# Optimization experiments

Hardware: AMD Instinct MI355X
Metric: run time of the kernel (lower is better)

The kernel has to match this reference:

```python
import jax, jax.numpy as jnp
import numpy as np

D = 192          # embed_dim
DI = 2 * D       # d_inner (Mamba expand=2)
R = 12           # dt_rank = ceil(D / d_state)
N = 16           # d_state
DEPTH = 24
P = 16           # patch size
B = 4
SS, TS = 256, 128
PT = (TS // P) ** 2   # 64 template patches
PS = (SS // P) ** 2   # 256 search patches
L = PT + PS + 1       # 321 tokens (middle cls)


def setup_inputs() -> dict:
    key = jax.random.key(0)
    ks = jax.random.split(key, 24)
    f = lambda k, shp, s=0.02: (jax.random.normal(k, shp) * s).astype(jnp.float32)
    Alog = jnp.log(jnp.arange(1, N + 1, dtype=jnp.float32))  # S4D-real init
    Alog = jnp.tile(Alog, (DEPTH, DI, 1))
    return {
        "x_search": f(ks[0], (B, 3, SS, SS), 1.0),
        "x_template": f(ks[1], (B, 3, TS, TS), 1.0),
        "patch_w": f(ks[2], (D, 3, P, P)),
        "patch_b": jnp.zeros((D,), jnp.float32),
        "cls_token": f(ks[3], (1, 1, D)),
        "pos_embed": f(ks[4], (1, L, D)),
        "Win": f(ks[5], (DEPTH, 2 * DI, D)),
        "convw": f(ks[6], (DEPTH, DI, 4), 0.2),
        "convb": jnp.zeros((DEPTH, DI), jnp.float32),
        "Wx": f(ks[7], (DEPTH, R + 2 * N, DI)),
        "Wdt": f(ks[8], (DEPTH, DI, R), 0.1),
        "bdt": f(ks[9], (DEPTH, DI), 0.1),
        "Alog": Alog,
        "Dp": jnp.ones((DEPTH, DI), jnp.float32),
        "convw_b": f(ks[10], (DEPTH, DI, 4), 0.2),
        "convb_b": jnp.zeros((DEPTH, DI), jnp.float32),
        "Wx_b": f(ks[11], (DEPTH, R + 2 * N, DI)),
        "Wdt_b": f(ks[12], (DEPTH, DI, R), 0.1),
        "bdt_b": f(ks[13], (DEPTH, DI), 0.1),
        "Alog_b": Alog,
        "Dp_b": jnp.ones((DEPTH, DI), jnp.float32),
        "Wout": f(ks[14], (DEPTH, D, DI)),
        "normw": jnp.ones((DEPTH, D), jnp.float32),
        "normw_f": jnp.ones((D,), jnp.float32),
    }


def silu(x):
    return x * jax.nn.sigmoid(x)


def rmsnorm(x, w, eps=1e-5):
    return x * jax.lax.rsqrt(jnp.mean(x * x, -1, keepdims=True) + eps) * w


def patch_embed(x, w, b):
    # non-overlapping patch conv == blocked reshape + einsum
    Bn, C, H, W = x.shape
    xp = x.reshape(Bn, C, H // P, P, W // P, P)
    t = jnp.einsum('bcipjq,dcpq->bijd', xp, w)
    return t.reshape(Bn, (H // P) * (W // P), -1) + b


def causal_conv(u, w, b):
    # depthwise causal conv, kernel 4: u [B,DI,L], w [DI,4]
    Lx = u.shape[-1]
    up = jnp.pad(u, ((0, 0), (0, 0), (3, 0)))
    y = sum(w[:, k][None, :, None] * up[:, :, k:k + Lx] for k in range(4))
    return y + b[None, :, None]


def selective_scan(u, delta, A, Bm, Cm, Dp):
    # u, delta: [B,DI,L]; A: [DI,N]; Bm, Cm: [B,N,L]
    dA = jnp.exp(jnp.einsum('bdl,dn->lbdn', delta, A))
    dBu = jnp.einsum('bdl,bnl->lbdn', delta * u, Bm)

    def step(h, inp):
        dAt, dBut, ct = inp
        h = dAt * h + dBut
        return h, jnp.einsum('bdn,bn->bd', h, ct)

    h0 = jnp.zeros((u.shape[0], DI, N), u.dtype)
    _, ys = jax.lax.scan(step, h0, (dA, dBu, Cm.transpose(2, 0, 1)))
    y = ys.transpose(1, 2, 0)  # [B,DI,L]
    return y + Dp[None, :, None] * u


def _branch(x, z, convw, convb, Wx, Wdt, bdt, Alog, Dp):
    xc = silu(causal_conv(x, convw, convb))
    xdbl = jnp.einsum('bdl,ed->ble', xc, Wx)
    dt, Bm, Cm = xdbl[..., :R], xdbl[..., R:R + N], xdbl[..., R + N:]
    delta = jax.nn.softplus(jnp.einsum('blr,dr->bdl', dt, Wdt) + bdt[None, :, None])
    y = selective_scan(xc, delta, -jnp.exp(Alog), Bm.transpose(0, 2, 1),
                       Cm.transpose(0, 2, 1), Dp)
    return y * silu(z)


def _mixer(h, p):
    xz = jnp.einsum('bld,ed->ble', h, p['Win'])
    x = xz[..., :DI].transpose(0, 2, 1)   # [B,DI,L]
    z = xz[..., DI:].transpose(0, 2, 1)
    y = _branch(x, z, p['convw'], p['convb'], p['Wx'], p['Wdt'], p['bdt'],
                p['Alog'], p['Dp'])
    yb = _branch(x[..., ::-1], z[..., ::-1], p['convw_b'], p['convb_b'], p['Wx_b'],
                 p['Wdt_b'], p['bdt_b'], p['Alog_b'], p['Dp_b'])
    out = (y + yb[..., ::-1]) * 0.5  # bimamba v2 with if_divide_out
    return jnp.einsum('bdl,od->blo', out, p['Wout'])


def reference(x_search, x_template, patch_w, patch_b, cls_token, pos_embed,
              Win, convw, convb, Wx, Wdt, bdt, Alog, Dp,
              convw_b, convb_b, Wx_b, Wdt_b, bdt_b, Alog_b, Dp_b,
              Wout, normw, normw_f):
    ts = patch_embed(x_template, patch_w, patch_b)   # [B,64,D]
    ss = patch_embed(x_search, patch_w, patch_b)     # [B,256,D]
    tok = jnp.concatenate([ts, ss], 1)               # [B,320,D]
    mid = tok.shape[1] // 2
    cls = jnp.broadcast_to(cls_token, (tok.shape[0], 1, D))
    tok = jnp.concatenate([tok[:, :mid], cls, tok[:, mid:]], 1) + pos_embed

    lp = {'Win': Win, 'convw': convw, 'convb': convb, 'Wx': Wx, 'Wdt': Wdt,
          'bdt': bdt, 'Alog': Alog, 'Dp': Dp, 'convw_b': convw_b,
          'convb_b': convb_b, 'Wx_b': Wx_b, 'Wdt_b': Wdt_b, 'bdt_b': bdt_b,
          'Alog_b': Alog_b, 'Dp_b': Dp_b, 'Wout': Wout, 'normw': normw}

    def layer_step(carry, p):
        hidden, residual = carry
        residual = hidden + residual           # add
        hn = rmsnorm(residual, p['normw'])     # norm (fused_add_norm semantics)
        hidden = _mixer(hn, p)                 # mamba mixer
        return (hidden, residual), None

    (hidden, residual), _ = jax.lax.scan(layer_step, (tok, jnp.zeros_like(tok)), lp)
    return rmsnorm(hidden + residual, normw_f)   # final add + norm, [B,321,D]
```

## Files before the change

kernel.cpp:

```cpp
#include <hip/hip_runtime.h>
#include <math.h>

#define B_ 4
#define L_ 321
#define D_ 192
#define DI_ 384
#define E_ 768
#define R_ 12
#define N_ 16
#define DEPTH_ 24
#define XD 44

#define NC_ 21
#define LC_ 16

typedef __attribute__((ext_vector_type(8))) short bf16x8;
typedef __attribute__((ext_vector_type(4))) float f32x4;
typedef unsigned short ushort_t;

__device__ __forceinline__ float silu_f(float x) { return x / (1.f + __expf(-x)); }

__device__ __forceinline__ ushort_t f2bf(float x) {
    union { float f; unsigned u; } v; v.f = x;
    return (ushort_t)((v.u + 0x7fffu + ((v.u >> 16) & 1u)) >> 16);
}
__device__ __forceinline__ float bf2f(ushort_t h) {
    union { unsigned u; float f; } v; v.u = ((unsigned)h) << 16; return v.f;
}

__global__ void cvt_bf16_multi(const float* __restrict__ s0, ushort_t* __restrict__ d0, int n0,
                               const float* __restrict__ s1, ushort_t* __restrict__ d1, int n1,
                               const float* __restrict__ s2, ushort_t* __restrict__ d2, int n2,
                               const float* __restrict__ s3, ushort_t* __restrict__ d3, int n3,
                               const float* __restrict__ s4, ushort_t* __restrict__ d4, int n4) {
    int total = n0 + n1 + n2 + n3 + n4;
    for (int i = blockIdx.x * blockDim.x + threadIdx.x; i < total; i += gridDim.x * blockDim.x) {
        int j = i;
// ... 7 lines not shown
                    if (j < n3) { s = s3; d = d3; }
                    else { j -= n3; s = s4; d = d4; }
                }
            }
        }
        d[j] = f2bf(s[j]);
    }
}

__global__ void im2col_kernel(const float* __restrict__ xs, const float* __restrict__ xt,
                              ushort_t* __restrict__ pm) {
    int p_all = blockIdx.x % 320;
    int b = blockIdx.x / 320;
    const float* src; int i, j, W;
    if (p_all < 64) { int p = p_all; i = p >> 3; j = p & 7; W = 128; src = xt + (size_t)b*3*128*128; }
    else            { int p = p_all - 64; i = p >> 4; j = p & 15; W = 256; src = xs + (size_t)b*3*256*256; }
    ushort_t* dst = pm + (size_t)blockIdx.x * 768;
    for (int m = threadIdx.x; m < 768; m += blockDim.x) {
        int c = m >> 8, rem = m & 255, pp = rem >> 4, qq = rem & 15;
        dst[m] = f2bf(src[(size_t)(c*W + i*16 + pp)*W + j*16 + qq]);
    }
}

__global__ void tok_rms(const float* __restrict__ tokmat, const float* __restrict__ pb,
                        const float* __restrict__ cls, const float* __restrict__ pos,
                        const float* __restrict__ normw,
                        float* __restrict__ residual, ushort_t* __restrict__ hn) {
    int blk = blockIdx.x;
    int b = blk / L_, t = blk % L_;
    int d = threadIdx.x;
    float v;
    if (t == 160) v = cls[d];
    else {
        int p = (t < 160) ? t : t - 1;
        v = tokmat[(size_t)(b*320 + p)*D_ + d] + pb[d];
    }
    v += pos[t*D_ + d];
    residual[(size_t)blk*D_ + d] = v;
    float sq = v * v;
#pragma unroll
    for (int m = 1; m < 64; m <<= 1) sq += __shfl_xor(sq, m, 64);
    __shared__ float part[3];
    int wave = d >> 6, lane = d & 63;
    if (lane == 0) part[wave] = sq;
    __syncthreads();
    float tot = part[0] + part[1] + part[2];
    float scale = rsqrtf(tot / (float)D_ + 1e-5f);
    hn[(size_t)blk*D_ + d] = f2bf(v * scale * normw[d]);
}

template<int WM, int WN, int MFR, int NFR, int CMODE>
__global__ __launch_bounds__(WM*WN*64) void mfma_gemm(const ushort_t* __restrict__ A,
                          const ushort_t* __restrict__ Bw,
                          float* __restrict__ Cf, ushort_t* __restrict__ Ch,
                          int M, int N, int K) {
    constexpr int BM = WM * MFR * 16;
    constexpr int BN = WN * NFR * 16;
    int bx = blockIdx.x, by = blockIdx.y;
    int wave = threadIdx.x >> 6, lane = threadIdx.x & 63;
    int wr = wave / WN, wc = wave % WN;
    int m0 = by * BM + wr * MFR * 16;
    int n0 = bx * BN + wc * NFR * 16;
    int lrow = lane & 15;
    int lk   = (lane >> 4) * 8;

    f32x4 acc[MFR][NFR];
#pragma unroll
    for (int i = 0; i < MFR; ++i)
#pragma unroll
        for (int j = 0; j < NFR; ++j) acc[i][j] = (f32x4){0.f, 0.f, 0.f, 0.f};

    for (int k0 = 0; k0 < K; k0 += 32) {
        bf16x8 a[MFR], b[NFR];
#pragma unroll
        for (int i = 0; i < MFR; ++i) {
            int r = m0 + i*16 + lrow; r = min(r, M - 1);
            a[i] = *(const bf16x8*)(A + (size_t)r*K + k0 + lk);
        }
#pragma unroll
        for (int jn = 0; jn < NFR; ++jn) {
            int c = n0 + jn*16 + lrow; c = min(c, N - 1);
            b[jn] = *(const bf16x8*)(Bw + (size_t)c*K + k0 + lk);
        }
#pragma unroll
        for (int i = 0; i < MFR; ++i)
#pragma unroll
            for (int jn = 0; jn < NFR; ++jn)
                acc[i][jn] = __builtin_amdgcn_mfma_f32_16x16x32_bf16(a[i], b[jn], acc[i][jn], 0, 0, 0);
    }

    int crow = (lane >> 4) * 4;
    int ccol = lane & 15;
#pragma unroll
    for (int i = 0; i < MFR; ++i)
#pragma unroll
        for (int jn = 0; jn < NFR; ++jn) {
            int c = n0 + jn*16 + ccol;
            if (c >= N) continue;
#pragma unroll
            for (int j = 0; j < 4; ++j) {
                int r = m0 + i*16 + crow + j;
                if (r < M) {
                    if (CMODE == 0) Cf[(size_t)r*N + c] = acc[i][jn][j];
                    else            Ch[(size_t)r*N + c] = f2bf(acc[i][jn][j]);
                }
            }
        }
}

__global__ void conv_kernel(const ushort_t* __restrict__ xz,
                            const float* __restrict__ cw, const float* __restrict__ cb,
                            const float* __restrict__ cwb, const float* __restrict__ cbb,
                            ushort_t* __restrict__ xc_f, ushort_t* __restrict__ xc_b) {
    int blk = blockIdx.x;
    int b = blk / L_, l = blk % L_;
    int d = threadIdx.x;
    const ushort_t* xbase = xz + (size_t)b*L_*E_ + d;
    float acc = cb[d];
#pragma unroll
    for (int k = 0; k < 4; ++k) {
        int t = l - 3 + k;
        if (t >= 0) acc = fmaf(cw[d*4 + k], bf2f(xbase[(size_t)t*E_]), acc);
    }
    xc_f[(size_t)(b*L_ + l)*DI_ + d] = f2bf(silu_f(acc));
    float accb = cbb[d];
#pragma unroll
    for (int k = 0; k < 4; ++k) {
        int t = l - 3 + k;
        if (t >= 0) accb = fmaf(cwb[d*4 + k], bf2f(xbase[(size_t)(L_ - 1 - t)*E_]), accb);
    }
    xc_b[(size_t)(b*L_ + l)*DI_ + d] = f2bf(silu_f(accb));
}

__global__ __launch_bounds__(384) void scan1_xdbl(
    const ushort_t* __restrict__ xc_f, const ushort_t* __restrict__ xc_b,
    const ushort_t* __restrict__ Wxf, const ushort_t* __restrict__ Wxbw,
    const float* __restrict__ Wdt, const float* __restrict__ bdt,
    const float* __restrict__ Wdtb, const float* __restrict__ bdtb,
    const float* __restrict__ Alog, const float* __restrict__ Alogb,
    float* __restrict__ xdbl_f, float* __restrict__ xdbl_b,
    float* __restrict__ hloc, float* __restrict__ aprod) {
    int c = blockIdx.x, b = blockIdx.y, br = blockIdx.z;
    int tid = threadIdx.x, wave = tid >> 6, lane = tid & 63;
    const ushort_t* xc = br ? xc_b : xc_f;
    const ushort_t* Wx = br ? Wxbw : Wxf;
    const float* Wd = br ? Wdtb : Wdt;
    const float* bd = br ? bdtb : bdt;
    const float* Al = br ? Alogb : Alog;
    float* xdout = br ? xdbl_b : xdbl_f;

    __shared__ float sxd[LC_][48];
    int lbeg = c * LC_;
    int len = min(lbeg + LC_, L_) - lbeg;

    if (wave < 3) {
        int lrow = lane & 15, lk = (lane >> 4) * 8;
        int arow = b * L_ + min(lbeg + lrow, L_ - 1);
        int bcol = min(wave * 16 + lrow, XD - 1);
        f32x4 acc = (f32x4){0.f, 0.f, 0.f, 0.f};
        for (int k0 = 0; k0 < DI_; k0 += 32) {
            bf16x8 a  = *(const bf16x8*)(xc + (size_t)arow * DI_ + k0 + lk);
            bf16x8 bw = *(const bf16x8*)(Wx + (size_t)bcol * DI_ + k0 + lk);
            acc = __builtin_amdgcn_mfma_f32_16x16x32_bf16(a, bw, acc, 0, 0, 0);
        }
        int crow = (lane >> 4) * 4, ccol = lane & 15;
#pragma unroll
        for (int j = 0; j < 4; ++j) sxd[crow + j][wave * 16 + ccol] = acc[j];
    }

    int d = tid;
    float u[LC_];
    if (len == LC_) {
#pragma unroll
        for (int l2 = 0; l2 < LC_; ++l2)
            u[l2] = bf2f(xc[((size_t)b*L_ + lbeg + l2)*DI_ + d]);
    }
    __syncthreads();

    for (int idx = tid; idx < len * XD; idx += 384) {
        int l2 = idx / XD, col = idx % XD;
        xdout[((size_t)b*L_ + lbeg + l2)*XD + col] = sxd[l2][col];
    }

    float wreg[R_];
#pragma unroll
    for (int r = 0; r < R_; ++r) wreg[r] = Wd[d*R_ + r];
    float bdv = bd[d];
    float a[N_];
#pragma unroll
    for (int n = 0; n < N_; ++n) a[n] = -__expf(Al[d*N_ + n]);
    float h[N_], ap[N_];
#pragma unroll
    for (int n = 0; n < N_; ++n) { h[n] = 0.f; ap[n] = 1.f; }

    auto step = [&](int l2, float uv) {
        float dacc = bdv;
#pragma unroll
        for (int r = 0; r < R_; ++r) dacc = fmaf(wreg[r], sxd[l2][r], dacc);
        float dv = fmaxf(dacc, 0.f) + log1pf(__expf(-fabsf(dacc)));
        float du = dv * uv;
#pragma unroll
        for (int n = 0; n < N_; ++n) {
            float e = __expf(dv * a[n]);
            h[n] = fmaf(e, h[n], du * sxd[l2][R_ + n]);
            ap[n] *= e;
        }
    };
    if (len == LC_) {
#pragma unroll 4
        for (int l2 = 0; l2 < LC_; ++l2) step(l2, u[l2]);
    } else {
        for (int l2 = 0; l2 < len; ++l2)
            step(l2, bf2f(xc[((size_t)b*L_ + lbeg + l2)*DI_ + d]));
    }
    size_t base = (((size_t)(b*2 + br)*NC_ + c)*N_)*DI_ + d;
#pragma unroll
    for (int n = 0; n < N_; ++n) {
        hloc[base + (size_t)n*DI_]  = h[n];
        aprod[base + (size_t)n*DI_] = ap[n];
    }
}

__global__ void scan_combine(const float* __restrict__ hloc, const float* __restrict__ aprod,
                             float* __restrict__ hin) {
    int g = blockIdx.x * blockDim.x + threadIdx.x;
    int bb = g / (N_ * DI_);
    int rem = g % (N_ * DI_);
    float hrun = 0.f;
    for (int c = 0; c < NC_; ++c) {
        size_t idx = ((size_t)bb*NC_ + c)*N_*DI_ + rem;
        hin[idx] = hrun;
        hrun = fmaf(aprod[idx], hrun, hloc[idx]);
    }
}

__global__ __launch_bounds__(192) void scan_part3(
                           const ushort_t* __restrict__ xc_f, const ushort_t* __restrict__ xc_b,
                           const float* __restrict__ xdbl_f, const float* __restrict__ xdbl_b,
                           const float* __restrict__ Wdt, const float* __restrict__ bdt,
                           const float* __restrict__ Wdtb, const float* __restrict__ bdtb,
                           const ushort_t* __restrict__ xz,
                           const float* __restrict__ Alog, const float* __restrict__ Alogb,
                           const float* __restrict__ Dpf, const float* __restrict__ Dpb,
                           const float* __restrict__ hin,
                           ushort_t* __restrict__ y_f, ushort_t* __restrict__ y_b) {
    int c = blockIdx.x, b = blockIdx.y >> 1, half = blockIdx.y & 1, br = blockIdx.z;
    int tid = threadIdx.x;
    int d = half * 192 + tid;
    const ushort_t* xc = br ? xc_b : xc_f;
    const float* xd = br ? xdbl_b : xdbl_f;
    const float* Wd = br ? Wdtb : Wdt;
    const float* bd = br ? bdtb : bdt;
    const float* Al = br ? Alogb : Alog;
    const float* Dpp = br ? Dpb : Dpf;
    ushort_t* y = br ? y_b : y_f;
    __shared__ float sdt[LC_][R_];
    __shared__ float sB[LC_][N_];
    __shared__ float sC[LC_][N_];
    int lbeg = c * LC_;
    int len = min(lbeg + LC_, L_) - lbeg;
    for (int idx = tid; idx < len*N_; idx += 192) {
        int l2 = idx >> 4, n = idx & 15;
        size_t row = (size_t)b*L_ + lbeg + l2;
        sB[l2][n] = xd[row*XD + R_ + n];
        sC[l2][n] = xd[row*XD + R_ + N_ + n];
    }
    for (int idx = tid; idx < len*R_; idx += 192) {
        int l2 = idx / R_, r = idx % R_;
        sdt[l2][r] = xd[((size_t)b*L_ + lbeg + l2)*XD + r];
    }
    __syncthreads();
    float wreg[R_];
#pragma unroll
    for (int r = 0; r < R_; ++r) wreg[r] = Wd[d*R_ + r];
    float bdv = bd[d];
    float a[N_];
#pragma unroll
    for (int n = 0; n < N_; ++n) a[n] = -__expf(Al[d*N_ + n]);
    float h[N_];
    size_t hbase = (((size_t)(b*2 + br)*NC_ + c)*N_)*DI_ + d;
#pragma unroll
    for (int n = 0; n < N_; ++n) h[n] = hin[hbase + (size_t)n*DI_];
    float dpv = Dpp[d];

    auto step = [&](int l2, float uv) {
        float dacc = bdv;
#pragma unroll
        for (int r = 0; r < R_; ++r) dacc = fmaf(wreg[r], sdt[l2][r], dacc);
        float dv = fmaxf(dacc, 0.f) + log1pf(__expf(-fabsf(dacc)));
        float du = dv * uv;
        float yv = 0.f;
#pragma unroll
        for (int n = 0; n < N_; ++n) {
            float e = __expf(dv * a[n]);
            h[n] = fmaf(e, h[n], du * sB[l2][n]);
            yv = fmaf(h[n], sC[l2][n], yv);
        }
        yv = fmaf(dpv, uv, yv);
        int lo = br ? (L_ - 1 - (lbeg + l2)) : (lbeg + l2);
        float zv = bf2f(xz[((size_t)b*L_ + lo)*E_ + DI_ + d]);
        y[((size_t)b*L_ + lo)*DI_ + d] = f2bf(yv * silu_f(zv));
    };
    if (len == LC_) {
        float u[LC_];
#pragma unroll
        for (int l2 = 0; l2 < LC_; ++l2)
            u[l2] = bf2f(xc[((size_t)b*L_ + lbeg + l2)*DI_ + d]);
#pragma unroll 4
        for (int l2 = 0; l2 < LC_; ++l2) step(l2, u[l2]);
    } else {
        for (int l2 = 0; l2 < len; ++l2)
            step(l2, bf2f(xc[((size_t)b*L_ + lbeg + l2)*DI_ + d]));
    }
}

template<bool LAST>
__global__ __launch_bounds__(256) void outproj_fused(
    const ushort_t* __restrict__ yf, const ushort_t* __restrict__ yb,
    const ushort_t* __restrict__ Ww,
    float* __restrict__ residual, const float* __restrict__ nw,
    ushort_t* __restrict__ hn, float* __restrict__ outp) {
    const int M = B_*L_, Nn = D_, K = DI_;
    int wave = threadIdx.x >> 6, lane = threadIdx.x & 63;
    int m0 = blockIdx.x * 16;
    int n0 = wave * 48;
    int lrow = lane & 15, lk = (lane >> 4) * 8;

    f32x4 acc[3];
#pragma unroll
    for (int jn = 0; jn < 3; ++jn) acc[jn] = (f32x4){0.f, 0.f, 0.f, 0.f};

    for (int k0 = 0; k0 < K; k0 += 32) {
        int r = min(m0 + lrow, M - 1);
        bf16x8 vf = *(const bf16x8*)(yf + (size_t)r*K + k0 + lk);
        bf16x8 vb = *(const bf16x8*)(yb + (size_t)r*K + k0 + lk);
        bf16x8 a;
#pragma unroll
        for (int j = 0; j < 8; ++j)
            a[j] = (short)f2bf(0.5f*(bf2f((ushort_t)vf[j]) + bf2f((ushort_t)vb[j])));
        bf16x8 b[3];
#pragma unroll
        for (int jn = 0; jn < 3; ++jn) {
            int c = n0 + jn*16 + lrow;
            b[jn] = *(const bf16x8*)(Ww + (size_t)c*K + k0 + lk);
        }
#pragma unroll
        for (int jn = 0; jn < 3; ++jn)
            acc[jn] = __builtin_amdgcn_mfma_f32_16x16x32_bf16(a, b[jn], acc[jn], 0, 0, 0);
    }

    int crow = (lane >> 4) * 4, ccol = lane & 15;
    float resv[4][3];
    float sq[4] = {0.f, 0.f, 0.f, 0.f};
#pragma unroll
    for (int j = 0; j < 4; ++j) {
        int r = m0 + crow + j;
        bool ok = r < M;
#pragma unroll
        for (int jn = 0; jn < 3; ++jn) {
            int c = n0 + jn*16 + ccol;
            float v = ok ? (residual[(size_t)r*Nn + c] + acc[jn][j]) : 0.f;
            resv[j][jn] = v;
            sq[j] = fmaf(v, v, sq[j]);
        }
    }
#pragma unroll
    for (int m = 1; m < 16; m <<= 1)
#pragma unroll
        for (int j = 0; j < 4; ++j) sq[j] += __shfl_xor(sq[j], m, 64);

    __shared__ float part[16][4];
    if (ccol == 0) {
#pragma unroll
        for (int j = 0; j < 4; ++j) part[crow + j][wave] = sq[j];
    }
    __syncthreads();
#pragma unroll
    for (int j = 0; j < 4; ++j) {
        int r = m0 + crow + j;
        if (r >= M) continue;
        int rt = crow + j;
        float tot = part[rt][0] + part[rt][1] + part[rt][2] + part[rt][3];
        float scale = rsqrtf(tot / (float)Nn + 1e-5f);
#pragma unroll
        for (int jn = 0; jn < 3; ++jn) {
            int c = n0 + jn*16 + ccol;
            float v = resv[j][jn];
            if (LAST) {
                outp[(size_t)r*Nn + c] = v * scale * nw[c];
            } else {
                residual[(size_t)r*Nn + c] = v;
                hn[(size_t)r*Nn + c] = f2bf(v * scale * nw[c]);
            }
        }
    }
}

extern "C" void kernel_launch(void* const* d_in, const int* in_sizes, int n_in,
                              void* d_out, int out_size, void* d_ws, size_t ws_size,
                              hipStream_t stream) {
    const float* xs     = (const float*)d_in[0];
    const float* xt     = (const float*)d_in[1];
    const float* pw     = (const float*)d_in[2];
    const float* pb     = (const float*)d_in[3];
    const float* cls    = (const float*)d_in[4];
    const float* pos    = (const float*)d_in[5];
    const float* Win    = (const float*)d_in[6];
    const float* convw  = (const float*)d_in[7];
    const float* convb  = (const float*)d_in[8];
    const float* Wx     = (const float*)d_in[9];
    const float* Wdt    = (const float*)d_in[10];
    const float* bdt    = (const float*)d_in[11];
    const float* Alog   = (const float*)d_in[12];
    const float* Dp     = (const float*)d_in[13];
    const float* convwb = (const float*)d_in[14];
    const float* convbb = (const float*)d_in[15];
    const float* Wxb    = (const float*)d_in[16];
// ... 21 lines not shown
    float*    xdbl_b   = alloc(BL * XD);
    ushort_t* y_f      = (ushort_t*)alloc(BL * DI_ / 2);
    ushort_t* y_b      = (ushort_t*)alloc(BL * DI_ / 2);
    float*    hloc     = alloc(CHNK);
    float*    aprod    = alloc(CHNK);
    float*    hin      = alloc(CHNK);
    ushort_t* pw_bf    = (ushort_t*)alloc((size_t)D_ * 768 / 2);
    ushort_t* Win_bf   = (ushort_t*)alloc((size_t)DEPTH_ * E_ * D_ / 2);
    ushort_t* Wx_bf    = (ushort_t*)alloc((size_t)DEPTH_ * XD * DI_ / 2);
    ushort_t* Wxb_bf   = (ushort_t*)alloc((size_t)DEPTH_ * XD * DI_ / 2);
    ushort_t* Wout_bf  = (ushort_t*)alloc((size_t)DEPTH_ * D_ * DI_ / 2);
    (void)ws_size; (void)in_sizes; (void)n_in; (void)out_size;

    cvt_bf16_multi<<<dim3(2048), dim3(256), 0, stream>>>(
        pw,   pw_bf,   D_ * 768,
        Win,  Win_bf,  DEPTH_ * E_ * D_,
        Wx,   Wx_bf,   DEPTH_ * XD * DI_,
        Wxb,  Wxb_bf,  DEPTH_ * XD * DI_,
        Wout, Wout_bf, DEPTH_ * D_ * DI_);

    ushort_t* pmat   = (ushort_t*)hloc;
    float*    tokmat = aprod;
    im2col_kernel<<<dim3(B_ * 320), dim3(256), 0, stream>>>(xs, xt, pmat);
    mfma_gemm<2, 2, 2, 2, 0><<<dim3(3, 20), dim3(256), 0, stream>>>(
        pmat, pw_bf, tokmat, nullptr, B_ * 320, D_, 768);
    tok_rms<<<dim3(B_ * L_), dim3(192), 0, stream>>>(tokmat, pb, cls, pos, normw, residual, hn_bf);

    for (int layer = 0; layer < DEPTH_; ++layer) {
        const ushort_t* Win_l  = Win_bf  + (size_t)layer * E_ * D_;
        const ushort_t* Wx_l   = Wx_bf   + (size_t)layer * XD * DI_;
        const ushort_t* Wxb_l  = Wxb_bf  + (size_t)layer * XD * DI_;
        const ushort_t* Wout_l = Wout_bf + (size_t)layer * D_ * DI_;
        const float* cw_l    = convw  + (size_t)layer * DI_ * 4;
        const float* cb_l    = convb  + (size_t)layer * DI_;
        const float* cwb_l   = convwb + (size_t)layer * DI_ * 4;
        const float* cbb_l   = convbb + (size_t)layer * DI_;
        const float* Wdt_l   = Wdt    + (size_t)layer * DI_ * R_;
        const float* Wdtb_l  = Wdtb   + (size_t)layer * DI_ * R_;
        const float* bdt_l   = bdt    + (size_t)layer * DI_;
        const float* bdtb_l  = bdtb   + (size_t)layer * DI_;
        const float* Alog_l  = Alog   + (size_t)layer * DI_ * N_;
        const float* Alogb_l = Alogb  + (size_t)layer * DI_ * N_;
        const float* Dp_l    = Dp     + (size_t)layer * DI_;
        const float* Dpb_l   = Dpb    + (size_t)layer * DI_;

        mfma_gemm<2, 2, 2, 2, 1><<<dim3(12, 21), dim3(256), 0, stream>>>(
            hn_bf, Win_l, nullptr, xzb_bf, (int)BL, E_, D_);
        conv_kernel<<<dim3((int)BL), dim3(DI_), 0, stream>>>(
            xzb_bf, cw_l, cb_l, cwb_l, cbb_l, xcf_bf, xcb_bf);
        scan1_xdbl<<<dim3(NC_, B_, 2), dim3(384), 0, stream>>>(
            xcf_bf, xcb_bf, Wx_l, Wxb_l, Wdt_l, bdt_l, Wdtb_l, bdtb_l,
            Alog_l, Alogb_l, xdbl_f, xdbl_b, hloc, aprod);
        scan_combine<<<dim3((B_*2*N_*DI_)/256), dim3(256), 0, stream>>>(hloc, aprod, hin);
        scan_part3<<<dim3(NC_, B_ * 2, 2), dim3(192), 0, stream>>>(
            xcf_bf, xcb_bf, xdbl_f, xdbl_b, Wdt_l, bdt_l, Wdtb_l, bdtb_l, xzb_bf,
            Alog_l, Alogb_l, Dp_l, Dpb_l, hin, y_f, y_b);
        if (layer < DEPTH_ - 1) {
            outproj_fused<false><<<dim3(81), dim3(256), 0, stream>>>(
                y_f, y_b, Wout_l, residual, normw + (size_t)(layer + 1) * D_, hn_bf, nullptr);
        } else {
            outproj_fused<true><<<dim3(81), dim3(256), 0, stream>>>(
                y_f, y_b, Wout_l, residual, normwf, nullptr, out);
        }
    }
}
```

Baseline: 1.783 ms.

## Fuse all per-layer Mamba kernels into one cooperative persistent kernel with grid syncs

Replaces the six kernel launches per layer (24 layers) with a single cooperative kernel of 252 blocks that runs every stage and separates stages with grid.sync(). The aim is to remove launch overhead and inter-kernel gaps, which dominate because each stage is small. In exchange every block waits at each grid barrier, and the fixed 384-thread blocks change tile shapes (for example, out-projection now spans 6 waves with 32 columns each), so some stages may lose occupancy or efficiency.

After: 6.142 ms. 3.45x slower.

```diff
diff --git a/kernel.cpp b/kernel.cpp
--- a/kernel.cpp
+++ b/kernel.cpp
@@ -1,5 +1,8 @@
 #include <hip/hip_runtime.h>
+#include <hip/hip_cooperative_groups.h>
 #include <math.h>
+
+namespace cg = cooperative_groups;
 
 #define B_ 4
 #define L_ 321
@@ -13,6 +16,9 @@
 
 #define NC_ 21
 #define LC_ 16
+
+#define GRID_ 252
+#define THR_ 384
 
 typedef __attribute__((ext_vector_type(8))) short bf16x8;
 typedef __attribute__((ext_vector_type(4))) float f32x4;
@@ -66,6 +72,55 @@
     }
 }
 
+__global__ __launch_bounds__(256) void patch_gemm(const ushort_t* __restrict__ A,
+                          const ushort_t* __restrict__ Bw, float* __restrict__ Cf,
+                          int M, int N, int K) {
+    int bx = blockIdx.x, by = blockIdx.y;
+    int wave = threadIdx.x >> 6, lane = threadIdx.x & 63;
+    int wr = wave >> 1, wc = wave & 1;
+    int m0 = by * 64 + wr * 32;
+    int n0 = bx * 64 + wc * 32;
+    int lrow = lane & 15, lk = (lane >> 4) * 8;
+
+    f32x4 acc[2][2];
+#pragma unroll
+    for (int i = 0; i < 2; ++i)
+#pragma unroll
+        for (int j = 0; j < 2; ++j) acc[i][j] = (f32x4){0.f, 0.f, 0.f, 0.f};
+
+    for (int k0 = 0; k0 < K; k0 += 32) {
+        bf16x8 a[2], b[2];
+#pragma unroll
+        for (int i = 0; i < 2; ++i) {
+            int r = min(m0 + i*16 + lrow, M - 1);
+            a[i] = *(const bf16x8*)(A + (size_t)r*K + k0 + lk);
+        }
+#pragma unroll
+        for (int jn = 0; jn < 2; ++jn) {
+            int c = min(n0 + jn*16 + lrow, N - 1);
+            b[jn] = *(const bf16x8*)(Bw + (size_t)c*K + k0 + lk);
+        }
+#pragma unroll
+        for (int i = 0; i < 2; ++i)
+#pragma unroll
+            for (int jn = 0; jn < 2; ++jn)
+                acc[i][jn] = __builtin_amdgcn_mfma_f32_16x16x32_bf16(a[i], b[jn], acc[i][jn], 0, 0, 0);
+    }
+    int crow = (lane >> 4) * 4, ccol = lane & 15;
+#pragma unroll
+    for (int i = 0; i < 2; ++i)
+#pragma unroll
+        for (int jn = 0; jn < 2; ++jn) {
+            int c = n0 + jn*16 + ccol;
+            if (c >= N) continue;
+#pragma unroll
+            for (int j = 0; j < 4; ++j) {
+                int r = m0 + i*16 + crow + j;
+                if (r < M) Cf[(size_t)r*N + c] = acc[i][jn][j];
+            }
+        }
+}
+
 __global__ void tok_rms(const float* __restrict__ tokmat, const float* __restrict__ pb,
                         const float* __restrict__ cls, const float* __restrict__ pos,
                         const float* __restrict__ normw,
@@ -93,350 +148,345 @@
     hn[(size_t)blk*D_ + d] = f2bf(v * scale * normw[d]);
 }
 
-template<int WM, int WN, int MFR, int NFR, int CMODE>
-__global__ __launch_bounds__(WM*WN*64) void mfma_gemm(const ushort_t* __restrict__ A,
-                          const ushort_t* __restrict__ Bw,
-                          float* __restrict__ Cf, ushort_t* __restrict__ Ch,
-                          int M, int N, int K) {
-    constexpr int BM = WM * MFR * 16;
-    constexpr int BN = WN * NFR * 16;
-    int bx = blockIdx.x, by = blockIdx.y;
-    int wave = threadIdx.x >> 6, lane = threadIdx.x & 63;
-    int wr = wave / WN, wc = wave % WN;
-    int m0 = by * BM + wr * MFR * 16;
-    int n0 = bx * BN + wc * NFR * 16;
-    int lrow = lane & 15;
-    int lk   = (lane >> 4) * 8;
-
-    f32x4 acc[MFR][NFR];
-#pragma unroll
-    for (int i = 0; i < MFR; ++i)
-#pragma unroll
-        for (int j = 0; j < NFR; ++j) acc[i][j] = (f32x4){0.f, 0.f, 0.f, 0.f};
-
-    for (int k0 = 0; k0 < K; k0 += 32) {
-        bf16x8 a[MFR], b[NFR];
-#pragma unroll
-        for (int i = 0; i < MFR; ++i) {
-            int r = m0 + i*16 + lrow; r = min(r, M - 1);
-            a[i] = *(const bf16x8*)(A + (size_t)r*K + k0 + lk);
-        }
-#pragma unroll
-        for (int jn = 0; jn < NFR; ++jn) {
-            int c = n0 + jn*16 + lrow; c = min(c, N - 1);
-            b[jn] = *(const bf16x8*)(Bw + (size_t)c*K + k0 + lk);
-        }
-#pragma unroll
-        for (int i = 0; i < MFR; ++i)
-#pragma unroll
-            for (int jn = 0; jn < NFR; ++jn)
-                acc[i][jn] = __builtin_amdgcn_mfma_f32_16x16x32_bf16(a[i], b[jn], acc[i][jn], 0, 0, 0);
-    }
-
-    int crow = (lane >> 4) * 4;
-    int ccol = lane & 15;
-#pragma unroll
-    for (int i = 0; i < MFR; ++i)
-#pragma unroll
-        for (int jn = 0; jn < NFR; ++jn) {
-            int c = n0 + jn*16 + ccol;
-            if (c >= N) continue;
+struct MegaArgs {
+    const ushort_t *Win_bf, *Wx_bf, *Wxb_bf, *Wout_bf;
+    const float *convw, *convb, *convwb, *convbb;
+    const float *Wdt, *bdt, *Wdtb, *bdtb;
+    const float *Alog, *Alogb, *Dp, *Dpb;
+    const float *normw, *normwf;
+    float *residual;
+    ushort_t *hn, *xzb, *xcf, *xcb;
+    float *xdbl_f, *xdbl_b;
+    ushort_t *yf, *yb;
+    float *hloc, *aprod, *hin;
+    float *out;
+};
+
+__global__ void __launch_bounds__(THR_) mega_kernel(MegaArgs A) {
+    cg::grid_group grid = cg::this_grid();
+    const int bid = blockIdx.x;
+    const int tid = threadIdx.x;
+    const int wave = tid >> 6, lane = tid & 63;
+    const int lrow = lane & 15, lk = (lane >> 4) * 8;
+    const int crow = (lane >> 4) * 4, ccol = lane & 15;
+    const int M = B_ * L_;
+
+    __shared__ union SM {
+        float sxd[LC_][48];
+        struct { float sdt[LC_][R_]; float sB[LC_][N_]; float sC[LC_][N_]; } p3;
+        float part[16][6];
+    } sm;
+
+    for (int layer = 0; layer < DEPTH_; ++layer) {
+        const ushort_t* Win_l  = A.Win_bf  + (size_t)layer * E_ * D_;
+        const ushort_t* Wx_l   = A.Wx_bf   + (size_t)layer * XD * DI_;
+        const ushort_t* Wxb_l  = A.Wxb_bf  + (size_t)layer * XD * DI_;
+        const ushort_t* Wout_l = A.Wout_bf + (size_t)layer * D_ * DI_;
+        const float* cw_l    = A.convw  + (size_t)layer * DI_ * 4;
+        const float* cb_l    = A.convb  + (size_t)layer * DI_;
+        const float* cwb_l   = A.convwb + (size_t)layer * DI_ * 4;
+        const float* cbb_l   = A.convbb + (size_t)layer * DI_;
+        const float* Wdt_l   = A.Wdt    + (size_t)layer * DI_ * R_;
+        const float* Wdtb_l  = A.Wdtb   + (size_t)layer * DI_ * R_;
+        const float* bdt_l   = A.bdt    + (size_t)layer * DI_;
+        const float* bdtb_l  = A.bdtb   + (size_t)layer * DI_;
+        const float* Alog_l  = A.Alog   + (size_t)layer * DI_ * N_;
+        const float* Alogb_l = A.Alogb  + (size_t)layer * DI_ * N_;
+        const float* Dp_l    = A.Dp     + (size_t)layer * DI_;
+        const float* Dpb_l   = A.Dpb    + (size_t)layer * DI_;
+
+        if (bid < 168) {
+            int bx = bid % 12, by = bid / 12;
+            int wr = wave >> 1, wc = wave & 1;
+            int m0 = by * 96 + wr * 32;
+            int n0 = bx * 64 + wc * 32;
+            f32x4 acc[2][2];
+#pragma unroll
+            for (int i = 0; i < 2; ++i)
+#pragma unroll
+                for (int j = 0; j < 2; ++j) acc[i][j] = (f32x4){0.f, 0.f, 0.f, 0.f};
+            for (int k0 = 0; k0 < D_; k0 += 32) {
+                bf16x8 a[2], bw[2];
+#pragma unroll
+                for (int i = 0; i < 2; ++i) {
+                    int r = min(m0 + i*16 + lrow, M - 1);
+                    a[i] = *(const bf16x8*)(A.hn + (size_t)r*D_ + k0 + lk);
+                }
+#pragma unroll
+                for (int j = 0; j < 2; ++j) {
+                    int c = n0 + j*16 + lrow;
+                    bw[j] = *(const bf16x8*)(Win_l + (size_t)c*D_ + k0 + lk);
+                }
+#pragma unroll
+                for (int i = 0; i < 2; ++i)
+#pragma unroll
+                    for (int j = 0; j < 2; ++j)
+                        acc[i][j] = __builtin_amdgcn_mfma_f32_16x16x32_bf16(a[i], bw[j], acc[i][j], 0, 0, 0);
+            }
+#pragma unroll
+            for (int i = 0; i < 2; ++i)
+#pragma unroll
+                for (int j = 0; j < 2; ++j) {
+                    int c = n0 + j*16 + ccol;
+#pragma unroll
+                    for (int jj = 0; jj < 4; ++jj) {
+                        int r = m0 + i*16 + crow + jj;
+                        if (r < M) A.xzb[(size_t)r*E_ + c] = f2bf(acc[i][j][jj]);
+                    }
+                }
+        }
+        grid.sync();
+
+        for (int idx = bid*THR_ + tid; idx < M*DI_; idx += GRID_*THR_) {
+            int row = idx / DI_, d = idx % DI_;
+            int b = row / L_, l = row % L_;
+            const ushort_t* xbase = A.xzb + (size_t)b*L_*E_ + d;
+            float acc = cb_l[d];
+#pragma unroll
+            for (int k = 0; k < 4; ++k) {
+                int t = l - 3 + k;
+                if (t >= 0) acc = fmaf(cw_l[d*4 + k], bf2f(xbase[(size_t)t*E_]), acc);
+            }
+            A.xcf[(size_t)row*DI_ + d] = f2bf(silu_f(acc));
+            float accb = cbb_l[d];
+#pragma unroll
+            for (int k = 0; k < 4; ++k) {
+                int t = l - 3 + k;
+                if (t >= 0) accb = fmaf(cwb_l[d*4 + k], bf2f(xbase[(size_t)(L_ - 1 - t)*E_]), accb);
+            }
+            A.xcb[(size_t)row*DI_ + d] = f2bf(silu_f(accb));
+        }
+        grid.sync();
+
+        if (bid < 168) {
+            int c = bid % NC_;
+            int g2 = bid / NC_;
+            int b = g2 >> 1, br = g2 & 1;
+            const ushort_t* xc = br ? A.xcb : A.xcf;
+            const ushort_t* Wx = br ? Wxb_l : Wx_l;
+            const float* Wd = br ? Wdtb_l : Wdt_l;
+            const float* bd = br ? bdtb_l : bdt_l;
+            const float* Al = br ? Alogb_l : Alog_l;
+            float* xdout = br ? A.xdbl_b : A.xdbl_f;
+            int lbeg = c * LC_;
+            int len = min(lbeg + LC_, L_) - lbeg;
+
+            if (wave < 3) {
+                int arow = b * L_ + min(lbeg + lrow, L_ - 1);
+                int bcol = min(wave * 16 + lrow, XD - 1);
+                f32x4 acc = (f32x4){0.f, 0.f, 0.f, 0.f};
+                for (int k0 = 0; k0 < DI_; k0 += 32) {
+                    bf16x8 a  = *(const bf16x8*)(xc + (size_t)arow * DI_ + k0 + lk);
+                    bf16x8 bw = *(const bf16x8*)(Wx + (size_t)bcol * DI_ + k0 + lk);
+                    acc = __builtin_amdgcn_mfma_f32_16x16x32_bf16(a, bw, acc, 0, 0, 0);
+                }
+#pragma unroll
+                for (int j = 0; j < 4; ++j) sm.sxd[crow + j][wave * 16 + ccol] = acc[j];
+            }
+            int d = tid;
+            float u[LC_];
+            if (len == LC_) {
+#pragma unroll
+                for (int l2 = 0; l2 < LC_; ++l2)
+                    u[l2] = bf2f(xc[((size_t)b*L_ + lbeg + l2)*DI_ + d]);
+            }
+            __syncthreads();
+            for (int idx = tid; idx < len * XD; idx += THR_) {
+                int l2 = idx / XD, col = idx % XD;
+                xdout[((size_t)b*L_ + lbeg + l2)*XD + col] = sm.sxd[l2][col];
+            }
+            float wreg[R_];
+#pragma unroll
+            for (int r = 0; r < R_; ++r) wreg[r] = Wd[d*R_ + r];
+            float bdv = bd[d];
+            float a[N_];
+#pragma unroll
+            for (int n = 0; n < N_; ++n) a[n] = -__expf(Al[d*N_ + n]);
+            float h[N_], ap[N_];
+#pragma unroll
+            for (int n = 0; n < N_; ++n) { h[n] = 0.f; ap[n] = 1.f; }
+            auto step = [&](int l2, float uv) {
+                float dacc = bdv;
+#pragma unroll
+                for (int r = 0; r < R_; ++r) dacc = fmaf(wreg[r], sm.sxd[l2][r], dacc);
+                float dv = fmaxf(dacc, 0.f) + log1pf(__expf(-fabsf(dacc)));
+                float du = dv * uv;
+#pragma unroll
+                for (int n = 0; n < N_; ++n) {
+                    float e = __expf(dv * a[n]);
+                    h[n] = fmaf(e, h[n], du * sm.sxd[l2][R_ + n]);
+                    ap[n] *= e;
+                }
+            };
+            if (len == LC_) {
+#pragma unroll 4
+                for (int l2 = 0; l2 < LC_; ++l2) step(l2, u[l2]);
+            } else {
+                for (int l2 = 0; l2 < len; ++l2)
+                    step(l2, bf2f(xc[((size_t)b*L_ + lbeg + l2)*DI_ + d]));
+            }
+            size_t base = (((size_t)(b*2 + br)*NC_ + c)*N_)*DI_ + d;
+#pragma unroll
+            for (int n = 0; n < N_; ++n) {
+                A.hloc[base + (size_t)n*DI_]  = h[n];
+                A.aprod[base + (size_t)n*DI_] = ap[n];
+            }
+        }
+        grid.sync();
+
+        if (bid < 128) {
+            int g = bid*THR_ + tid;
+            int bb = g / (N_ * DI_);
+            int rem = g % (N_ * DI_);
+            float hrun = 0.f;
+            for (int c = 0; c < NC_; ++c) {
+                size_t idx = ((size_t)bb*NC_ + c)*N_*DI_ + rem;
+                A.hin[idx] = hrun;
+                hrun = fmaf(A.aprod[idx], hrun, A.hloc[idx]);
+            }
+        }
+        grid.sync();
+
+        if (bid < 168) {
+            int c = bid % NC_;
+            int g2 = bid / NC_;
+            int b = g2 >> 1, br = g2 & 1;
+            const ushort_t* xc = br ? A.xcb : A.xcf;
+            const float* xd = br ? A.xdbl_b : A.xdbl_f;
+            const float* Wd = br ? Wdtb_l : Wdt_l;
+            const float* bd = br ? bdtb_l : bdt_l;
+            const float* Al = br ? Alogb_l : Alog_l;
+            const float* Dpp = br ? Dpb_l : Dp_l;
+            ushort_t* y = br ? A.yb : A.yf;
+            int lbeg = c * LC_;
+            int len = min(lbeg + LC_, L_) - lbeg;
+            for (int idx = tid; idx < len*N_; idx += THR_) {
+                int l2 = idx >> 4, n = idx & 15;
+                size_t row = (size_t)b*L_ + lbeg + l2;
+                sm.p3.sB[l2][n] = xd[row*XD + R_ + n];
+                sm.p3.sC[l2][n] = xd[row*XD + R_ + N_ + n];
+            }
+            for (int idx = tid; idx < len*R_; idx += THR_) {
+                int l2 = idx / R_, r = idx % R_;
+                sm.p3.sdt[l2][r] = xd[((size_t)b*L_ + lbeg + l2)*XD + r];
+            }
+            __syncthreads();
+            int d = tid;
+            float wreg[R_];
+#pragma unroll
+            for (int r = 0; r < R_; ++r) wreg[r] = Wd[d*R_ + r];
+            float bdv = bd[d];
+            float a[N_];
+#pragma unroll
+            for (int n = 0; n < N_; ++n) a[n] = -__expf(Al[d*N_ + n]);
+            float h[N_];
+            size_t hbase = (((size_t)(b*2 + br)*NC_ + c)*N_)*DI_ + d;
+#pragma unroll
+            for (int n = 0; n < N_; ++n) h[n] = A.hin[hbase + (size_t)n*DI_];
+            float dpv = Dpp[d];
+            auto step = [&](int l2, float uv) {
+                float dacc = bdv;
+#pragma unroll
+                for (int r = 0; r < R_; ++r) dacc = fmaf(wreg[r], sm.p3.sdt[l2][r], dacc);
+                float dv = fmaxf(dacc, 0.f) + log1pf(__expf(-fabsf(dacc)));
+                float du = dv * uv;
+                float yv = 0.f;
+#pragma unroll
+                for (int n = 0; n < N_; ++n) {
+                    float e = __expf(dv * a[n]);
+                    h[n] = fmaf(e, h[n], du * sm.p3.sB[l2][n]);
+                    yv = fmaf(h[n], sm.p3.sC[l2][n], yv);
+                }
+                yv = fmaf(dpv, uv, yv);
+                int lo = br ? (L_ - 1 - (lbeg + l2)) : (lbeg + l2);
+                float zv = bf2f(A.xzb[((size_t)b*L_ + lo)*E_ + DI_ + d]);
+                y[((size_t)b*L_ + lo)*DI_ + d] = f2bf(yv * silu_f(zv));
+            };
+            if (len == LC_) {
+                float u[LC_];
+#pragma unroll
+                for (int l2 = 0; l2 < LC_; ++l2)
+                    u[l2] = bf2f(xc[((size_t)b*L_ + lbeg + l2)*DI_ + d]);
+#pragma unroll 4
+                for (int l2 = 0; l2 < LC_; ++l2) step(l2, u[l2]);
+            } else {
+                for (int l2 = 0; l2 < len; ++l2)
+                    step(l2, bf2f(xc[((size_t)b*L_ + lbeg + l2)*DI_ + d]));
+            }
+        }
+        grid.sync();
+
+        if (bid < 81) {
+            bool last = (layer == DEPTH_ - 1);
+            const float* nw = last ? A.normwf : (A.normw + (size_t)(layer + 1) * D_);
+            int m0 = bid * 16;
+            int n0 = wave * 32;
+            f32x4 acc[2];
+#pragma unroll
+            for (int jn = 0; jn < 2; ++jn) acc[jn] = (f32x4){0.f, 0.f, 0.f, 0.f};
+            for (int k0 = 0; k0 < DI_; k0 += 32) {
+                int r = min(m0 + lrow, M - 1);
+                bf16x8 vf = *(const bf16x8*)(A.yf + (size_t)r*DI_ + k0 + lk);
+                bf16x8 vb = *(const bf16x8*)(A.yb + (size_t)r*DI_ + k0 + lk);
+                bf16x8 a;
+#pragma unroll
+                for (int j = 0; j < 8; ++j)
+                    a[j] = (short)f2bf(0.5f*(bf2f((ushort_t)vf[j]) + bf2f((ushort_t)vb[j])));
+                bf16x8 b[2];
+#pragma unroll
+                for (int jn = 0; jn < 2; ++jn) {
+                    int c = n0 + jn*16 + lrow;
+                    b[jn] = *(const bf16x8*)(Wout_l + (size_t)c*DI_ + k0 + lk);
+                }
+#pragma unroll
+                for (int jn = 0; jn < 2; ++jn)
+                    acc[jn] = __builtin_amdgcn_mfma_f32_16x16x32_bf16(a, b[jn], acc[jn], 0, 0, 0);
+            }
+            float resv[4][2];
+            float sq[4] = {0.f, 0.f, 0.f, 0.f};
 #pragma unroll
             for (int j = 0; j < 4; ++j) {
-                int r = m0 + i*16 + crow + j;
-                if (r < M) {
-                    if (CMODE == 0) Cf[(size_t)r*N + c] = acc[i][jn][j];
-                    else            Ch[(size_t)r*N + c] = f2bf(acc[i][jn][j]);
-                }
-            }
-        }
-}
-
-__global__ void conv_kernel(const ushort_t* __restrict__ xz,
-                            const float* __restrict__ cw, const float* __restrict__ cb,
-                            const float* __restrict__ cwb, const float* __restrict__ cbb,
-                            ushort_t* __restrict__ xc_f, ushort_t* __restrict__ xc_b) {
-    int blk = blockIdx.x;
-    int b = blk / L_, l = blk % L_;
-    int d = threadIdx.x;
-    const ushort_t* xbase = xz + (size_t)b*L_*E_ + d;
-    float acc = cb[d];
-#pragma unroll
-    for (int k = 0; k < 4; ++k) {
-        int t = l - 3 + k;
-        if (t >= 0) acc = fmaf(cw[d*4 + k], bf2f(xbase[(size_t)t*E_]), acc);
-    }
-    xc_f[(size_t)(b*L_ + l)*DI_ + d] = f2bf(silu_f(acc));
-    float accb = cbb[d];
-#pragma unroll
-    for (int k = 0; k < 4; ++k) {
-        int t = l - 3 + k;
-        if (t >= 0) accb = fmaf(cwb[d*4 + k], bf2f(xbase[(size_t)(L_ - 1 - t)*E_]), accb);
-    }
-    xc_b[(size_t)(b*L_ + l)*DI_ + d] = f2bf(silu_f(accb));
-}
-
-__global__ __launch_bounds__(384) void scan1_xdbl(
-    const ushort_t* __restrict__ xc_f, const ushort_t* __restrict__ xc_b,
-    const ushort_t* __restrict__ Wxf, const ushort_t* __restrict__ Wxbw,
-    const float* __restrict__ Wdt, const float* __restrict__ bdt,
-    const float* __restrict__ Wdtb, const float* __restrict__ bdtb,
-    const float* __restrict__ Alog, const float* __restrict__ Alogb,
-    float* __restrict__ xdbl_f, float* __restrict__ xdbl_b,
-    float* __restrict__ hloc, float* __restrict__ aprod) {
-    int c = blockIdx.x, b = blockIdx.y, br = blockIdx.z;
-    int tid = threadIdx.x, wave = tid >> 6, lane = tid & 63;
-    const ushort_t* xc = br ? xc_b : xc_f;
-    const ushort_t* Wx = br ? Wxbw : Wxf;
-    const float* Wd = br ? Wdtb : Wdt;
-    const float* bd = br ? bdtb : bdt;
-    const float* Al = br ? Alogb : Alog;
-    float* xdout = br ? xdbl_b : xdbl_f;
-
-    __shared__ float sxd[LC_][48];
-    int lbeg = c * LC_;
-    int len = min(lbeg + LC_, L_) - lbeg;
-
-    if (wave < 3) {
-        int lrow = lane & 15, lk = (lane >> 4) * 8;
-        int arow = b * L_ + min(lbeg + lrow, L_ - 1);
-        int bcol = min(wave * 16 + lrow, XD - 1);
-        f32x4 acc = (f32x4){0.f, 0.f, 0.f, 0.f};
-        for (int k0 = 0; k0 < DI_; k0 += 32) {
-            bf16x8 a  = *(const bf16x8*)(xc + (size_t)arow * DI_ + k0 + lk);
-            bf16x8 bw = *(const bf16x8*)(Wx + (size_t)bcol * DI_ + k0 + lk);
-            acc = __builtin_amdgcn_mfma_f32_16x16x32_bf16(a, bw, acc, 0, 0, 0);
-        }
-        int crow = (lane >> 4) * 4, ccol = lane & 15;
-#pragma unroll
-        for (int j = 0; j < 4; ++j) sxd[crow + j][wave * 16 + ccol] = acc[j];
-    }
-
-    int d = tid;
-    float u[LC_];
-    if (len == LC_) {
-#pragma unroll
-        for (int l2 = 0; l2 < LC_; ++l2)
-            u[l2] = bf2f(xc[((size_t)b*L_ + lbeg + l2)*DI_ + d]);
-    }
-    __syncthreads();
-
-    for (int idx = tid; idx < len * XD; idx += 384) {
-        int l2 = idx / XD, col = idx % XD;
-        xdout[((size_t)b*L_ + lbeg + l2)*XD + col] = sxd[l2][col];
-    }
-
-    float wreg[R_];
-#pragma unroll
-    for (int r = 0; r < R_; ++r) wreg[r] = Wd[d*R_ + r];
-    float bdv = bd[d];
-    float a[N_];
-#pragma unroll
-    for (int n = 0; n < N_; ++n) a[n] = -__expf(Al[d*N_ + n]);
-    float h[N_], ap[N_];
-#pragma unroll
-    for (int n = 0; n < N_; ++n) { h[n] = 0.f; ap[n] = 1.f; }
-
-    auto step = [&](int l2, float uv) {
-        float dacc = bdv;
-#pragma unroll
-        for (int r = 0; r < R_; ++r) dacc = fmaf(wreg[r], sxd[l2][r], dacc);
-        float dv = fmaxf(dacc, 0.f) + log1pf(__expf(-fabsf(dacc)));
-        float du = dv * uv;
-#pragma unroll
-        for (int n = 0; n < N_; ++n) {
-            float e = __expf(dv * a[n]);
-            h[n] = fmaf(e, h[n], du * sxd[l2][R_ + n]);
-            ap[n] *= e;
-        }
-    };
-    if (len == LC_) {
-#pragma unroll 4
-        for (int l2 = 0; l2 < LC_; ++l2) step(l2, u[l2]);
-    } else {
-        for (int l2 = 0; l2 < len; ++l2)
-            step(l2, bf2f(xc[((size_t)b*L_ + lbeg + l2)*DI_ + d]));
-    }
-    size_t base = (((size_t)(b*2 + br)*NC_ + c)*N_)*DI_ + d;
-#pragma unroll
-    for (int n = 0; n < N_; ++n) {
-        hloc[base + (size_t)n*DI_]  = h[n];
-        aprod[base + (size_t)n*DI_] = ap[n];
-    }
-}
-
-__global__ void scan_combine(const float* __restrict__ hloc, const float* __restrict__ aprod,
-                             float* __restrict__ hin) {
-    int g = blockIdx.x * blockDim.x + threadIdx.x;
-    int bb = g / (N_ * DI_);
-    int rem = g % (N_ * DI_);
-    float hrun = 0.f;
-    for (int c = 0; c < NC_; ++c) {
-        size_t idx = ((size_t)bb*NC_ + c)*N_*DI_ + rem;
-        hin[idx] = hrun;
-        hrun = fmaf(aprod[idx], hrun, hloc[idx]);
-    }
-}
-
-__global__ __launch_bounds__(192) void scan_part3(
-                           const ushort_t* __restrict__ xc_f, const ushort_t* __restrict__ xc_b,
-                           const float* __restrict__ xdbl_f, const float* __restrict__ xdbl_b,
-                           const float* __restrict__ Wdt, const float* __restrict__ bdt,
-                           const float* __restrict__ Wdtb, const float* __restrict__ bdtb,
-                           const ushort_t* __restrict__ xz,
-                           const float* __restrict__ Alog, const float* __restrict__ Alogb,
-                           const float* __restrict__ Dpf, const float* __restrict__ Dpb,
-                           const float* __restrict__ hin,
-                           ushort_t* __restrict__ y_f, ushort_t* __restrict__ y_b) {
-    int c = blockIdx.x, b = blockIdx.y >> 1, half = blockIdx.y & 1, br = blockIdx.z;
-    int tid = threadIdx.x;
-    int d = half * 192 + tid;
-    const ushort_t* xc = br ? xc_b : xc_f;
-    const float* xd = br ? xdbl_b : xdbl_f;
-    const float* Wd = br ? Wdtb : Wdt;
-    const float* bd = br ? bdtb : bdt;
-    const float* Al = br ? Alogb : Alog;
-    const float* Dpp = br ? Dpb : Dpf;
-    ushort_t* y = br ? y_b : y_f;
-    __shared__ float sdt[LC_][R_];
-    __shared__ float sB[LC_][N_];
-    __shared__ float sC[LC_][N_];
-    int lbeg = c * LC_;
-    int len = min(lbeg + LC_, L_) - lbeg;
-    for (int idx = tid; idx < len*N_; idx += 192) {
-        int l2 = idx >> 4, n = idx & 15;
-        size_t row = (size_t)b*L_ + lbeg + l2;
-        sB[l2][n] = xd[row*XD + R_ + n];
-        sC[l2][n] = xd[row*XD + R_ + N_ + n];
-    }
-    for (int idx = tid; idx < len*R_; idx += 192) {
-        int l2 = idx / R_, r = idx % R_;
-        sdt[l2][r] = xd[((size_t)b*L_ + lbeg + l2)*XD + r];
-    }
-    __syncthreads();
-    float wreg[R_];
-#pragma unroll
-    for (int r = 0; r < R_; ++r) wreg[r] = Wd[d*R_ + r];
-    float bdv = bd[d];
-    float a[N_];
-#pragma unroll
-    for (int n = 0; n < N_; ++n) a[n] = -__expf(Al[d*N_ + n]);
-    float h[N_];
-    size_t hbase = (((size_t)(b*2 + br)*NC_ + c)*N_)*DI_ + d;
-#pragma unroll
-    for (int n = 0; n < N_; ++n) h[n] = hin[hbase + (size_t)n*DI_];
-    float dpv = Dpp[d];
-
-    auto step = [&](int l2, float uv) {
-        float dacc = bdv;
-#pragma unroll
-        for (int r = 0; r < R_; ++r) dacc = fmaf(wreg[r], sdt[l2][r], dacc);
-        float dv = fmaxf(dacc, 0.f) + log1pf(__expf(-fabsf(dacc)));
-        float du = dv * uv;
-        float yv = 0.f;
-#pragma unroll
-        for (int n = 0; n < N_; ++n) {
-            float e = __expf(dv * a[n]);
-            h[n] = fmaf(e, h[n], du * sB[l2][n]);
-            yv = fmaf(h[n], sC[l2][n], yv);
-        }
-        yv = fmaf(dpv, uv, yv);
-        int lo = br ? (L_ - 1 - (lbeg + l2)) : (lbeg + l2);
-        float zv = bf2f(xz[((size_t)b*L_ + lo)*E_ + DI_ + d]);
-        y[((size_t)b*L_ + lo)*DI_ + d] = f2bf(yv * silu_f(zv));
-    };
-    if (len == LC_) {
-        float u[LC_];
-#pragma unroll
-        for (int l2 = 0; l2 < LC_; ++l2)
-            u[l2] = bf2f(xc[((size_t)b*L_ + lbeg + l2)*DI_ + d]);
-#pragma unroll 4
-        for (int l2 = 0; l2 < LC_; ++l2) step(l2, u[l2]);
-    } else {
-        for (int l2 = 0; l2 < len; ++l2)
-            step(l2, bf2f(xc[((size_t)b*L_ + lbeg + l2)*DI_ + d]));
-    }
-}
-
-template<bool LAST>
-__global__ __launch_bounds__(256) void outproj_fused(
-    const ushort_t* __restrict__ yf, const ushort_t* __restrict__ yb,
-    const ushort_t* __restrict__ Ww,
-    float* __restrict__ residual, const float* __restrict__ nw,
-    ushort_t* __restrict__ hn, float* __restrict__ outp) {
-    const int M = B_*L_, Nn = D_, K = DI_;
-    int wave = threadIdx.x >> 6, lane = threadIdx.x & 63;
-    int m0 = blockIdx.x * 16;
-    int n0 = wave * 48;
-    int lrow = lane & 15, lk = (lane >> 4) * 8;
-
-    f32x4 acc[3];
-#pragma unroll
-    for (int jn = 0; jn < 3; ++jn) acc[jn] = (f32x4){0.f, 0.f, 0.f, 0.f};
-
-    for (int k0 = 0; k0 < K; k0 += 32) {
-        int r = min(m0 + lrow, M - 1);
-        bf16x8 vf = *(const bf16x8*)(yf + (size_t)r*K + k0 + lk);
-        bf16x8 vb = *(const bf16x8*)(yb + (size_t)r*K + k0 + lk);
-        bf16x8 a;
-#pragma unroll
-        for (int j = 0; j < 8; ++j)
-            a[j] = (short)f2bf(0.5f*(bf2f((ushort_t)vf[j]) + bf2f((ushort_t)vb[j])));
-        bf16x8 b[3];
-#pragma unroll
-        for (int jn = 0; jn < 3; ++jn) {
-            int c = n0 + jn*16 + lrow;
-            b[jn] = *(const bf16x8*)(Ww + (size_t)c*K + k0 + lk);
-        }
-#pragma unroll
-        for (int jn = 0; jn < 3; ++jn)
-            acc[jn] = __builtin_amdgcn_mfma_f32_16x16x32_bf16(a, b[jn], acc[jn], 0, 0, 0);
-    }
-
-    int crow = (lane >> 4) * 4, ccol = lane & 15;
-    float resv[4][3];
-    float sq[4] = {0.f, 0.f, 0.f, 0.f};
-#pragma unroll
-    for (int j = 0; j < 4; ++j) {
-        int r = m0 + crow + j;
-        bool ok = r < M;
-#pragma unroll
-        for (int jn = 0; jn < 3; ++jn) {
-            int c = n0 + jn*16 + ccol;
-            float v = ok ? (residual[(size_t)r*Nn + c] + acc[jn][j]) : 0.f;
-            resv[j][jn] = v;
-            sq[j] = fmaf(v, v, sq[j]);
-        }
-    }
-#pragma unroll
-    for (int m = 1; m < 16; m <<= 1)
-#pragma unroll
-        for (int j = 0; j < 4; ++j) sq[j] += __shfl_xor(sq[j], m, 64);
-
-    __shared__ float part[16][4];
-    if (ccol == 0) {
-#pragma unroll
-        for (int j = 0; j < 4; ++j) part[crow + j][wave] = sq[j];
-    }
-    __syncthreads();
-#pragma unroll
-    for (int j = 0; j < 4; ++j) {
-        int r = m0 + crow + j;
-        if (r >= M) continue;
-        int rt = crow + j;
-        float tot = part[rt][0] + part[rt][1] + part[rt][2] + part[rt][3];
-        float scale = rsqrtf(tot / (float)Nn + 1e-5f);
-#pragma unroll
-        for (int jn = 0; jn < 3; ++jn) {
-            int c = n0 + jn*16 + ccol;
-            float v = resv[j][jn];
-            if (LAST) {
-                outp[(size_t)r*Nn + c] = v * scale * nw[c];
-            } else {
-                residual[(size_t)r*Nn + c] = v;
-                hn[(size_t)r*Nn + c] = f2bf(v * scale * nw[c]);
-            }
-        }
+                int r = m0 + crow + j;
+                bool ok = r < M;
+#pragma unroll
+                for (int jn = 0; jn < 2; ++jn) {
+                    int c = n0 + jn*16 + ccol;
+                    float v = ok ? (A.residual[(size_t)r*D_ + c] + acc[jn][j]) : 0.f;
+                    resv[j][jn] = v;
+                    sq[j] = fmaf(v, v, sq[j]);
+                }
+            }
+#pragma unroll
+            for (int m = 1; m < 16; m <<= 1)
+#pragma unroll
+                for (int j = 0; j < 4; ++j) sq[j] += __shfl_xor(sq[j], m, 64);
+            if (ccol == 0) {
+#pragma unroll
+                for (int j = 0; j < 4; ++j) sm.part[crow + j][wave] = sq[j];
+            }
+            __syncthreads();
+#pragma unroll
+            for (int j = 0; j < 4; ++j) {
+                int r = m0 + crow + j;
+                if (r >= M) continue;
+                int rt = crow + j;
+                float tot = sm.part[rt][0] + sm.part[rt][1] + sm.part[rt][2]
+                          + sm.part[rt][3] + sm.part[rt][4] + sm.part[rt][5];
+                float scale = rsqrtf(tot / (float)D_ + 1e-5f);
+#pragma unroll
+                for (int jn = 0; jn < 2; ++jn) {
+                    int c = n0 + jn*16 + ccol;
+                    float v = resv[j][jn];
+                    if (last) {
+                        A.out[(size_t)r*D_ + c] = v * scale * nw[c];
+                    } else {
+                        A.residual[(size_t)r*D_ + c] = v;
+                        A.hn[(size_t)r*D_ + c] = f2bf(v * scale * nw[c]);
+                    }
+                }
+            }
+        }
+        grid.sync();
     }
 }
 
@@ -504,45 +554,22 @@
     ushort_t* pmat   = (ushort_t*)hloc;
     float*    tokmat = aprod;
     im2col_kernel<<<dim3(B_ * 320), dim3(256), 0, stream>>>(xs, xt, pmat);
-    mfma_gemm<2, 2, 2, 2, 0><<<dim3(3, 20), dim3(256), 0, stream>>>(
-        pmat, pw_bf, tokmat, nullptr, B_ * 320, D_, 768);
+    patch_gemm<<<dim3(3, 20), dim3(256), 0, stream>>>(pmat, pw_bf, tokmat, B_ * 320, D_, 768);
     tok_rms<<<dim3(B_ * L_), dim3(192), 0, stream>>>(tokmat, pb, cls, pos, normw, residual, hn_bf);
 
-    for (int layer = 0; layer < DEPTH_; ++layer) {
-        const ushort_t* Win_l  = Win_bf  + (size_t)layer * E_ * D_;
-        const ushort_t* Wx_l   = Wx_bf   + (size_t)layer * XD * DI_;
-        const ushort_t* Wxb_l  = Wxb_bf  + (size_t)layer * XD * DI_;
-        const ushort_t* Wout_l = Wout_bf + (size_t)layer * D_ * DI_;
-        const float* cw_l    = convw  + (size_t)layer * DI_ * 4;
-        const float* cb_l    = convb  + (size_t)layer * DI_;
-        const float* cwb_l   = convwb + (size_t)layer * DI_ * 4;
-        const float* cbb_l   = convbb + (size_t)layer * DI_;
-        const float* Wdt_l   = Wdt    + (size_t)layer * DI_ * R_;
-        const float* Wdtb_l  = Wdtb   + (size_t)layer * DI_ * R_;
-        const float* bdt_l   = bdt    + (size_t)layer * DI_;
-        const float* bdtb_l  = bdtb   + (size_t)layer * DI_;
-        const float* Alog_l  = Alog   + (size_t)layer * DI_ * N_;
-        const float* Alogb_l = Alogb  + (size_t)layer * DI_ * N_;
-        const float* Dp_l    = Dp     + (size_t)layer * DI_;
-        const float* Dpb_l   = Dpb    + (size_t)layer * DI_;
-
-        mfma_gemm<2, 2, 2, 2, 1><<<dim3(12, 21), dim3(256), 0, stream>>>(
-            hn_bf, Win_l, nullptr, xzb_bf, (int)BL, E_, D_);
-        conv_kernel<<<dim3((int)BL), dim3(DI_), 0, stream>>>(
-            xzb_bf, cw_l, cb_l, cwb_l, cbb_l, xcf_bf, xcb_bf);
-        scan1_xdbl<<<dim3(NC_, B_, 2), dim3(384), 0, stream>>>(
-            xcf_bf, xcb_bf, Wx_l, Wxb_l, Wdt_l, bdt_l, Wdtb_l, bdtb_l,
-            Alog_l, Alogb_l, xdbl_f, xdbl_b, hloc, aprod);
-        scan_combine<<<dim3((B_*2*N_*DI_)/256), dim3(256), 0, stream>>>(hloc, aprod, hin);
-        scan_part3<<<dim3(NC_, B_ * 2, 2), dim3(192), 0, stream>>>(
-            xcf_bf, xcb_bf, xdbl_f, xdbl_b, Wdt_l, bdt_l, Wdtb_l, bdtb_l, xzb_bf,
-            Alog_l, Alogb_l, Dp_l, Dpb_l, hin, y_f, y_b);
-        if (layer < DEPTH_ - 1) {
-            outproj_fused<false><<<dim3(81), dim3(256), 0, stream>>>(
-                y_f, y_b, Wout_l, residual, normw + (size_t)(layer + 1) * D_, hn_bf, nullptr);
-        } else {
-            outproj_fused<true><<<dim3(81), dim3(256), 0, stream>>>(
-                y_f, y_b, Wout_l, residual, normwf, nullptr, out);
-        }
-    }
-}
+    MegaArgs ma;
+    ma.Win_bf = Win_bf; ma.Wx_bf = Wx_bf; ma.Wxb_bf = Wxb_bf; ma.Wout_bf = Wout_bf;
+    ma.convw = convw; ma.convb = convb; ma.convwb = convwb; ma.convbb = convbb;
+    ma.Wdt = Wdt; ma.bdt = bdt; ma.Wdtb = Wdtb; ma.bdtb = bdtb;
+    ma.Alog = Alog; ma.Alogb = Alogb; ma.Dp = Dp; ma.Dpb = Dpb;
+    ma.normw = normw; ma.normwf = normwf;
+    ma.residual = residual;
+    ma.hn = hn_bf; ma.xzb = xzb_bf; ma.xcf = xcf_bf; ma.xcb = xcb_bf;
+    ma.xdbl_f = xdbl_f; ma.xdbl_b = xdbl_b;
+    ma.yf = y_f; ma.yb = y_b;
+    ma.hloc = hloc; ma.aprod = aprod; ma.hin = hin;
+    ma.out = out;
+    void* kargs[] = { &ma };
+    (void)hipLaunchCooperativeKernel((const void*)mega_kernel, dim3(GRID_), dim3(THR_),
+                                     kargs, 0, stream);
+}
```
